# Optimization experiments

Hardware: AMD Instinct MI355X
Metric: run time of the kernel (lower is better)

Reference implementation:

```python
import jax, jax.numpy as jnp
import numpy as np

B, S, D, H = 4, 1024, 1024, 16
DK = D // H
EPS = 1e-6

def setup_inputs() -> dict:
    key = jax.random.key(0)
    ks = jax.random.split(key, 7)
    scale = 1.0 / np.sqrt(D)
    return {
        "query": jax.random.normal(ks[0], (B, S, D), jnp.float32),
        "key": jax.random.normal(ks[1], (B, S, D), jnp.float32),
        "value": jax.random.normal(ks[2], (B, S, D), jnp.float32),
        "Wq": jax.random.normal(ks[3], (D, D), jnp.float32) * scale,
        "Wk": jax.random.normal(ks[4], (D, D), jnp.float32) * scale,
        "Wv": jax.random.normal(ks[5], (D, D), jnp.float32) * scale,
        "Wo": jax.random.normal(ks[6], (D, D), jnp.float32) * scale,
        "ln_gamma": jnp.ones((D,), jnp.float32),
        "ln_beta": jnp.zeros((D,), jnp.float32),
    }

def reference(query, key, value, Wq, Wk, Wv, Wo, ln_gamma, ln_beta):
    residual = query
    # projections (torch Linear: x @ W.T); reshape to [B,H,S,DK]
    def proj(x, W):
        y = jnp.einsum('bsd,ed->bse', x, W)
        return y.reshape(B, S, H, DK).transpose(0, 2, 1, 3)
    q, k, v = proj(query, Wq), proj(key, Wk), proj(value, Wv)
    scores = jnp.einsum('bhqd,bhkd->bhqk', q, k) / jnp.sqrt(jnp.float32(DK))
    p = jax.nn.softmax(scores, axis=-1)
    x = jnp.einsum('bhqk,bhkd->bhqd', p, v)
    x = x.transpose(0, 2, 1, 3).reshape(B, S, D)
    x = jnp.einsum('bsd,ed->bse', x, Wo)
    x = x + residual
    mu = jnp.mean(x, axis=-1, keepdims=True)
    var = jnp.var(x, axis=-1, keepdims=True)
    x = (x - mu) / jnp.sqrt(var + EPS) * ln_gamma + ln_beta
    return x
```

## Files before the change

### kernel.cpp

```cpp
#include <hip/hip_runtime.h>
#include <hip/hip_bf16.h>

#define B_ 4
#define S_ 1024
#define D_ 1024
#define H_ 16
#define DK_ 64
#define MROWS (B_*S_)

typedef short bf16x8 __attribute__((ext_vector_type(8)));
typedef float f32x4 __attribute__((ext_vector_type(4)));
typedef unsigned short u16;
typedef unsigned u32;
typedef u16 u16x4 __attribute__((ext_vector_type(4)));

__device__ __forceinline__ u16 f2bf(float f) {
    union { float f; unsigned u; } v; v.f = f;
    unsigned u = v.u;
    u += 0x7fff + ((u >> 16) & 1);
    return (u16)(u >> 16);
}

__device__ __forceinline__ void gld_lds16(const u16* gp, u16* lp) {
    __builtin_amdgcn_global_load_lds(
        (const __attribute__((address_space(1))) void*)gp,
        (__attribute__((address_space(3))) void*)lp,
        16, 0, 0);
}

__global__ __launch_bounds__(256) void pack_bf16(
    const float* __restrict__ q, const float* __restrict__ k, const float* __restrict__ v,
    const float* __restrict__ wq, const float* __restrict__ wk,
    const float* __restrict__ wv, const float* __restrict__ wo,
    u16* __restrict__ act_dst, u16* __restrict__ w_dst)
{
    const int NACT = 3 * MROWS * D_;
    const int NW   = 4 * D_ * D_;
    for (int c = blockIdx.x * blockDim.x + threadIdx.x;
         c < (NACT + NW) / 4; c += gridDim.x * blockDim.x) {
        int e = c * 4;
        const float* s; u16* d;
        if (e < NACT) {
            int t = e >> 22;
            int off = e & (4194304 - 1);
            s = (t == 0 ? q : t == 1 ? k : v) + off;
            d = act_dst + e;
        } else {
            int e2 = e - NACT;
            int t = e2 >> 20;
            int off = e2 & (1048576 - 1);
            s = (t == 0 ? wq : t == 1 ? wk : t == 2 ? wv : wo) + off;
            d = w_dst + e2;
        }
        float4 tv = *(const float4*)s;
        u16x4 o; o[0]=f2bf(tv.x); o[1]=f2bf(tv.y); o[2]=f2bf(tv.z); o[3]=f2bf(tv.w);
        *(u16x4*)d = o;
    }
}

template<int BM, bool EPI_RESID, bool VT>
__global__ __launch_bounds__(256) void gemm_fast(
    const u16* __restrict__ Ab, const u16* __restrict__ Wb,
    u16* __restrict__ Cb, float* __restrict__ Cf, const float* __restrict__ resid)
{
    constexpr int WN = (BM == 128) ? 2 : 4;
    constexpr int WCOLS = 128 / WN;
    constexpr int NR = WCOLS / 16;
    __shared__ u16 ldsA[BM * 64];
    __shared__ u16 ldsB[128 * 64];

    const int gx = gridDim.x, gy = gridDim.y, gz = gridDim.z;
    const int nwg = gx * gy * gz;
    const int flat = blockIdx.x + gx * (blockIdx.y + gy * blockIdx.z);
    const int f = (flat & 7) * (nwg >> 3) + (flat >> 3);
    const int bx = f % gx;
    const int rem = f / gx;
    const int by = rem % gy;
    const int z = rem / gy;

    Ab += (size_t)z * MROWS * D_;
    Wb += (size_t)z * D_ * D_;
    const u16* CbT = Cb + (EPI_RESID ? 0 : (size_t)z * MROWS * D_);
    u16* Cbz = (u16*)CbT;

    const int tid = threadIdx.x, lane = tid & 63, wid = tid >> 6;
    const int wr = (BM == 128) ? (wid >> 1) : 0;
    const int wc = (BM == 128) ? (wid & 1) : wid;
    const int m0 = by * BM, n0 = bx * 128;
    const int wbase = wid * 64;

    f32x4 acc[4][NR] = {};

    for (int kt = 0; kt < 1024; kt += 64) {
        __syncthreads();
        #pragma unroll
        for (int j = 0; j < BM / 32; ++j) {
            int ch = j * 256 + tid;
            int row = ch >> 3, c8 = (ch & 7) ^ (row & 7);
            gld_lds16(Ab + (size_t)(m0 + row) * 1024 + kt + c8 * 8,
                      &ldsA[(j * 256 + wbase) * 8]);
        }
        #pragma unroll
        for (int j = 0; j < 4; ++j) {
            int ch = j * 256 + tid;
            int row = ch >> 3, c8 = (ch & 7) ^ (row & 7);
            gld_lds16(Wb + (size_t)(n0 + row) * 1024 + kt + c8 * 8,
                      &ldsB[(j * 256 + wbase) * 8]);
        }
        __syncthreads();

        #pragma unroll
        for (int ks = 0; ks < 2; ++ks) {
            const int cb = ks * 32 + (lane >> 4) * 8;
            bf16x8 af[4], bfr[NR];
            #pragma unroll
            for (int m = 0; m < 4; ++m) {
                int row = wr * 64 + m * 16 + (lane & 15);
                af[m] = *(const bf16x8*)(&ldsA[row * 64 + (cb ^ ((row & 7) << 3))]);
            }
            #pragma unroll
            for (int n = 0; n < NR; ++n) {
                int row = wc * WCOLS + n * 16 + (lane & 15);
                bfr[n] = *(const bf16x8*)(&ldsB[row * 64 + (cb ^ ((row & 7) << 3))]);
            }
            #pragma unroll
            for (int m = 0; m < 4; ++m)
                #pragma unroll
                for (int n = 0; n < NR; ++n)
                    acc[m][n] = __builtin_amdgcn_mfma_f32_16x16x32_bf16(
                        af[m], bfr[n], acc[m][n], 0, 0, 0);
        }
    }

    if (VT && z == 2) {
        #pragma unroll
        for (int m = 0; m < 4; ++m)
            #pragma unroll
            for (int n = 0; n < NR; ++n) {
                u16x4 o;
                #pragma unroll
                for (int r = 0; r < 4; ++r) o[r] = f2bf(acc[m][n][r]);
                int grow = m0 + wr * 64 + m * 16 + (lane >> 4) * 4;
                int gcol = n0 + wc * WCOLS + n * 16 + (lane & 15);
                *(u16x4*)(&Cbz[(size_t)gcol * MROWS + grow]) = o;
            }
    } else {
        #pragma unroll
        for (int m = 0; m < 4; ++m)
            #pragma unroll
            for (int n = 0; n < NR; ++n)
                #pragma unroll
                for (int r = 0; r < 4; ++r) {
                    int grow = m0 + wr * 64 + m * 16 + (lane >> 4) * 4 + r;
                    int gcol = n0 + wc * WCOLS + n * 16 + (lane & 15);
                    if (EPI_RESID)
                        Cf[(size_t)grow * 1024 + gcol] = acc[m][n][r] + resid[(size_t)grow * 1024 + gcol];
                    else
                        Cbz[(size_t)grow * 1024 + gcol] = f2bf(acc[m][n][r]);
                }
    }
}

template<bool A_BF16, bool EPI_RESID>
__global__ __launch_bounds__(256) void gemm_bt(
    const void* __restrict__ Av, const float* __restrict__ Bw,
    u16* __restrict__ Cb, float* __restrict__ Cf,
    const float* __restrict__ resid, int M, int N, int K)
{
    __shared__ u16 lds[2][128 * 64];
    const int tid  = threadIdx.x;
    const int lane = tid & 63;
    const int wid  = tid >> 6;
    const int wr = wid >> 1, wc = wid & 1;
    const int m0 = blockIdx.y * 128, n0 = blockIdx.x * 128;

    f32x4 acc[4][4] = {};

    for (int kt = 0; kt < K; kt += 64) {
        #pragma unroll
        for (int j = 0; j < 8; ++j) {
            int idx4 = tid + 256 * j;
            int r = idx4 >> 4;
            int c = (idx4 & 15) * 4;
            u16x4 aw, bw;
            if (A_BF16) {
                const u16* Ab2 = (const u16*)Av;
                aw = *(const u16x4*)(Ab2 + (size_t)(m0 + r) * K + kt + c);
            } else {
                const float* Af = (const float*)Av;
                float4 t = *(const float4*)(Af + (size_t)(m0 + r) * K + kt + c);
                aw[0] = f2bf(t.x); aw[1] = f2bf(t.y); aw[2] = f2bf(t.z); aw[3] = f2bf(t.w);
            }
            {
                float4 t = *(const float4*)(Bw + (size_t)(n0 + r) * K + kt + c);
                bw[0] = f2bf(t.x); bw[1] = f2bf(t.y); bw[2] = f2bf(t.z); bw[3] = f2bf(t.w);
            }
            int sa = r * 64 + (c ^ ((r & 7) << 3));
            *(u16x4*)(&lds[0][sa]) = aw;
            *(u16x4*)(&lds[1][sa]) = bw;
        }
        __syncthreads();
        #pragma unroll
        for (int ks = 0; ks < 2; ++ks) {
            const int cb = ks * 32 + (lane >> 4) * 8;
            bf16x8 af[4], bfr[4];
            #pragma unroll
            for (int m = 0; m < 4; ++m) {
                int row = wr * 64 + m * 16 + (lane & 15);
                af[m] = *(const bf16x8*)(&lds[0][row * 64 + (cb ^ ((row & 7) << 3))]);
            }
            #pragma unroll
            for (int n = 0; n < 4; ++n) {
                int row = wc * 64 + n * 16 + (lane & 15);
                bfr[n] = *(const bf16x8*)(&lds[1][row * 64 + (cb ^ ((row & 7) << 3))]);
            }
            #pragma unroll
            for (int m = 0; m < 4; ++m)
                #pragma unroll
                for (int n = 0; n < 4; ++n)
                    acc[m][n] = __builtin_amdgcn_mfma_f32_16x16x32_bf16(
                        af[m], bfr[n], acc[m][n], 0, 0, 0);
        }
        __syncthreads();
    }

    #pragma unroll
    for (int m = 0; m < 4; ++m)
        #pragma unroll
        for (int n = 0; n < 4; ++n)
            #pragma unroll
            for (int r = 0; r < 4; ++r) {
                int grow = m0 + wr * 64 + m * 16 + (lane >> 4) * 4 + r;
                int gcol = n0 + wc * 64 + n * 16 + (lane & 15);
                float v = acc[m][n][r];
                if (EPI_RESID)
                    Cf[(size_t)grow * N + gcol] = v + resid[(size_t)grow * N + gcol];
                else
                    Cb[(size_t)grow * N + gcol] = f2bf(v);
            }
}

__global__ __launch_bounds__(512, 4) void attn_fwd6(
    const u16* __restrict__ Qg, const u16* __restrict__ Kg,
    const u16* __restrict__ Vt, u16* __restrict__ Og)
{
    __shared__ u16 ks2[64 * 64];
    __shared__ u16 vsT[64 * 64];
    __shared__ u16 ps[128 * 64];

    const int tid = threadIdx.x, lane = tid & 63, w = tid >> 6;
    const int g = lane >> 4, ql = lane & 15;

    const int bid = blockIdx.x;
    const int f = (bid & 7) * 64 + (bid >> 3);
    const int qt = f & 7, h = (f >> 3) & 15, b = f >> 7;
    const int q0 = qt * 128;
    const size_t rbase = (size_t)b * S_;
    const int cb0 = h * DK_;

    bf16x8 qb[2];
    {
        const u16* qp = Qg + (rbase + q0 + w * 16 + ql) * D_ + cb0 + 8 * g;
        qb[0] = *(const bf16x8*)(qp);
        qb[1] = *(const bf16x8*)(qp + 32);
    }

    auto stage_k = [&](int kv0) {
        int row = tid >> 3, c8 = (tid & 7) ^ (row & 7);
        gld_lds16(Kg + (rbase + kv0 + row) * D_ + cb0 + c8 * 8, &ks2[w * 512]);
    };
    auto stage_v = [&](int kv0) {
        int row = tid >> 3, c8 = (tid & 7) ^ (row & 7);
        gld_lds16(Vt + (size_t)(cb0 + row) * MROWS + rbase + kv0 + c8 * 8, &vsT[w * 512]);
    };

    stage_k(0);
    stage_v(0);
    __syncthreads();

    float mrow = -1e30f, lrow = 0.f;
    f32x4 xacc[4] = {};

    for (int jt = 0; jt < 16; ++jt) {
        f32x4 sacc[4] = {};
        __builtin_amdgcn_s_setprio(1);
        #pragma unroll
        for (int ks = 0; ks < 2; ++ks) {
            #pragma unroll
            for (int n = 0; n < 4; ++n) {
                int krow = n * 16 + ql;
                int c = 32 * ks + 8 * g;
                bf16x8 kf = *(const bf16x8*)(&ks2[krow * 64 + (c ^ ((krow & 7) << 3))]);
                sacc[n] = __builtin_amdgcn_mfma_f32_16x16x32_bf16(kf, qb[ks], sacc[n], 0, 0, 0);
            }
        }
        __builtin_amdgcn_s_setprio(0);

        __syncthreads();
        if (jt < 15) stage_k((jt + 1) * 64);

        float mt = sacc[0][0];
        #pragma unroll
        for (int n = 0; n < 4; ++n)
            #pragma unroll
            for (int r = 0; r < 4; ++r) mt = fmaxf(mt, sacc[n][r]);
        mt = fmaxf(mt, __shfl_xor(mt, 16));
        mt = fmaxf(mt, __shfl_xor(mt, 32));
        if (!__all(mt * 0.125f - mrow <= 8.f)) {
            float mnew = fmaxf(mrow, mt * 0.125f);
            float alpha = __expf(mrow - mnew);
            mrow = mnew;
            lrow *= alpha;
            #pragma unroll
            for (int r = 0; r < 4; ++r) {
                float a_r = __shfl(alpha, 4 * g + r);
                #pragma unroll
                for (int n2 = 0; n2 < 4; ++n2) xacc[n2][r] *= a_r;
            }
        }
        float rsum = 0.f;
        u16 pb[16];
        #pragma unroll
        for (int n = 0; n < 4; ++n)
            #pragma unroll
            for (int r = 0; r < 4; ++r) {
                float p = __expf(sacc[n][r] * 0.125f - mrow);
                rsum += p;
                pb[n * 4 + r] = f2bf(p);
            }
        rsum += __shfl_xor(rsum, 16);
        rsum += __shfl_xor(rsum, 32);
        lrow += rsum;

        {
            const int q = w * 16 + ql;
            #pragma unroll
            for (int n = 0; n < 4; ++n) {
                int c = 16 * n + 4 * g;
                *(u16x4*)(&ps[q * 64 + (c ^ ((q & 7) << 3))]) = *(const u16x4*)(&pb[n * 4]);
            }
        }
        asm volatile("s_waitcnt lgkmcnt(0)" ::: "memory");
        __builtin_amdgcn_sched_barrier(0);

        bf16x8 pa[2];
        {
            const int q = w * 16 + ql;
            #pragma unroll
            for (int ks = 0; ks < 2; ++ks) {
                int c = 32 * ks + 8 * g;
                pa[ks] = *(const bf16x8*)(&ps[q * 64 + (c ^ ((q & 7) << 3))]);
            }
        }

        __builtin_amdgcn_s_setprio(1);
        #pragma unroll
        for (int ks = 0; ks < 2; ++ks)
            #pragma unroll
            for (int n2 = 0; n2 < 4; ++n2) {
                int vrow = n2 * 16 + ql;
                int c2 = 32 * ks + 8 * g;
                bf16x8 bv = *(const bf16x8*)(&vsT[vrow * 64 + (c2 ^ ((vrow & 7) << 3))]);
                xacc[n2] = __builtin_amdgcn_mfma_f32_16x16x32_bf16(pa[ks], bv, xacc[n2], 0, 0, 0);
            }
        __builtin_amdgcn_s_setprio(0);

        __syncthreads();
        if (jt < 15) stage_v((jt + 1) * 64);
    }

    float linv[4];
    #pragma unroll
    for (int r = 0; r < 4; ++r) linv[r] = 1.f / __shfl(lrow, 4 * g + r);
    #pragma unroll
    for (int n2 = 0; n2 < 4; ++n2)
        #pragma unroll
        for (int r = 0; r < 4; ++r) {
            int qrow = q0 + w * 16 + 4 * g + r;
            int col = cb0 + n2 * 16 + ql;
            Og[(rbase + qrow) * D_ + col] = f2bf(xacc[n2][r] * linv[r]);
        }
}

__global__ __launch_bounds__(256) void attn_fwd(
    const u16* __restrict__ Qg, const u16* __restrict__ Kg,
    const u16* __restrict__ Vg, u16* __restrict__ Og)
{
    __shared__ u16 qs[64 * 64], ks2[64 * 64], vt[64 * 64], ps[64 * 64];
    const int tid = threadIdx.x, lane = tid & 63, w = tid >> 6;
    const int b = blockIdx.z, h = blockIdx.y, q0 = blockIdx.x * 64;
    const size_t rbase = (size_t)b * S_;
    const int cb0 = h * DK_;

    #pragma unroll
    for (int j = 0; j < 4; ++j) {
        int idx4 = tid + 256 * j;
        int r = idx4 >> 4, c = (idx4 & 15) * 4;
        u16x4 t = *(const u16x4*)(Qg + (rbase + q0 + r) * D_ + cb0 + c);
        *(u16x4*)(&qs[r * 64 + (c ^ ((r & 7) << 3))]) = t;
    }

    float mrow[4], lrow[4];
    f32x4 xacc[4] = {};
    #pragma unroll
    for (int r = 0; r < 4; ++r) { mrow[r] = -1e30f; lrow[r] = 0.f; }

    for (int jt = 0; jt < 16; ++jt) {
        const int kv0 = jt * 64;
        __syncthreads();
        #pragma unroll
        for (int j = 0; j < 4; ++j) {
            int idx4 = tid + 256 * j;
            int r = idx4 >> 4, c = (idx4 & 15) * 4;
            u16x4 t = *(const u16x4*)(Kg + (rbase + kv0 + r) * D_ + cb0 + c);
            *(u16x4*)(&ks2[r * 64 + (c ^ ((r & 7) << 3))]) = t;
            u16x4 tv = *(const u16x4*)(Vg + (rbase + kv0 + r) * D_ + cb0 + c);
            #pragma unroll
            for (int jj = 0; jj < 4; ++jj) {
                int d = c + jj;
                vt[d * 64 + (r ^ ((d & 7) << 3))] = tv[jj];
            }
        }
        __syncthreads();

        f32x4 sacc[4] = {};
        #pragma unroll
        for (int ks = 0; ks < 2; ++ks) {
            const int cb = ks * 32 + (lane >> 4) * 8;
            int qrow = w * 16 + (lane & 15);
            bf16x8 aq = *(const bf16x8*)(&qs[qrow * 64 + (cb ^ ((qrow & 7) << 3))]);
            #pragma unroll
            for (int n = 0; n < 4; ++n) {
                int krow = n * 16 + (lane & 15);
                bf16x8 bk = *(const bf16x8*)(&ks2[krow * 64 + (cb ^ ((krow & 7) << 3))]);
                sacc[n] = __builtin_amdgcn_mfma_f32_16x16x32_bf16(aq, bk, sacc[n], 0, 0, 0);
            }
        }

        #pragma unroll
        for (int r = 0; r < 4; ++r) {
            float mx = fmaxf(fmaxf(sacc[0][r], sacc[1][r]),
                             fmaxf(sacc[2][r], sacc[3][r]));
            mx = fmaxf(mx, __shfl_xor(mx, 1));
            mx = fmaxf(mx, __shfl_xor(mx, 2));
            mx = fmaxf(mx, __shfl_xor(mx, 4));
            mx = fmaxf(mx, __shfl_xor(mx, 8));
            float mnew = fmaxf(mrow[r], mx * 0.125f);
            float alpha = __expf(mrow[r] - mnew);
            float p[4], rsum = 0.f;
            #pragma unroll
            for (int n = 0; n < 4; ++n) { p[n] = __expf(sacc[n][r] * 0.125f - mnew); rsum += p[n]; }
            rsum += __shfl_xor(rsum, 1);
            rsum += __shfl_xor(rsum, 2);
            rsum += __shfl_xor(rsum, 4);
            rsum += __shfl_xor(rsum, 8);
            lrow[r] = lrow[r] * alpha + rsum;
            mrow[r] = mnew;
            int qrow = w * 16 + (lane >> 4) * 4 + r;
            #pragma unroll
            for (int n = 0; n < 4; ++n) {
                xacc[n][r] *= alpha;
                int col = n * 16 + (lane & 15);
                ps[qrow * 64 + (col ^ ((qrow & 7) << 3))] = f2bf(p[n]);
            }
        }
        __syncthreads();

        #pragma unroll
        for (int ks = 0; ks < 2; ++ks) {
            const int cb = ks * 32 + (lane >> 4) * 8;
            int prow = w * 16 + (lane & 15);
            bf16x8 ap = *(const bf16x8*)(&ps[prow * 64 + (cb ^ ((prow & 7) << 3))]);
            #pragma unroll
            for (int n = 0; n < 4; ++n) {
                int vrow = n * 16 + (lane & 15);
                bf16x8 bv = *(const bf16x8*)(&vt[vrow * 64 + (cb ^ ((vrow & 7) << 3))]);
                xacc[n] = __builtin_amdgcn_mfma_f32_16x16x32_bf16(ap, bv, xacc[n], 0, 0, 0);
            }
        }
    }

    #pragma unroll
    for (int n = 0; n < 4; ++n)
        #pragma unroll
        for (int r = 0; r < 4; ++r) {
            int qrow = q0 + w * 16 + (lane >> 4) * 4 + r;
            int col = cb0 + n * 16 + (lane & 15);
            Og[(rbase + qrow) * D_ + col] = f2bf(xacc[n][r] / lrow[r]);
        }
}

__global__ __launch_bounds__(256) void ln_inplace(
    float* __restrict__ Y, const float* __restrict__ g, const float* __restrict__ bt)
{
    __shared__ float red[2][4];
    const int row = blockIdx.x, tid = threadIdx.x;
    float4 v = *(const float4*)(Y + (size_t)row * D_ + tid * 4);
    float s = v.x + v.y + v.z + v.w;
    float q = v.x * v.x + v.y * v.y + v.z * v.z + v.w * v.w;
    #pragma unroll
    for (int m = 1; m < 64; m <<= 1) { s += __shfl_xor(s, m); q += __shfl_xor(q, m); }
    const int w = tid >> 6, lane = tid & 63;
    if (lane == 0) { red[0][w] = s; red[1][w] = q; }
    __syncthreads();
    s = red[0][0] + red[0][1] + red[0][2] + red[0][3];
    q = red[1][0] + red[1][1] + red[1][2] + red[1][3];
    float mu = s * (1.f / 1024.f);
    float var = q * (1.f / 1024.f) - mu * mu;
    float rstd = rsqrtf(var + 1e-6f);
    float4 gv = *(const float4*)(g + tid * 4);
    float4 bv = *(const float4*)(bt + tid * 4);
    v.x = (v.x - mu) * rstd * gv.x + bv.x;
    v.y = (v.y - mu) * rstd * gv.y + bv.y;
    v.z = (v.z - mu) * rstd * gv.z + bv.z;
    v.w = (v.w - mu) * rstd * gv.w + bv.w;
    *(float4*)(Y + (size_t)row * D_ + tid * 4) = v;
}

extern "C" void kernel_launch(void* const* d_in, const int* in_sizes, int n_in,
                              void* d_out, int out_size, void* d_ws, size_t ws_size,
                              hipStream_t stream)
{
    const float* query = (const float*)d_in[0];
    const float* key   = (const float*)d_in[1];
    const float* value = (const float*)d_in[2];
    const float* Wq    = (const float*)d_in[3];
    const float* Wk    = (const float*)d_in[4];
    const float* Wv    = (const float*)d_in[5];
    const float* Wo    = (const float*)d_in[6];
    const float* gamma = (const float*)d_in[7];
    const float* beta  = (const float*)d_in[8];
    float* out = (float*)d_out;

    const size_t ACT = (size_t)MROWS * D_;
    const size_t WSZ = (size_t)D_ * D_;
    const size_t NEED = (3 * ACT + 4 * WSZ + 3 * ACT) * 2;

    if (ws_size >= NEED) {
        u16* actb = (u16*)d_ws;
        u16* wb   = actb + 3 * ACT;
        u16* pb   = wb + 4 * WSZ;
        u16* Ap   = actb;

        pack_bf16<<<2048, 256, 0, stream>>>(query, key, value, Wq, Wk, Wv, Wo, actb, wb);
        gemm_fast<128, false, true><<<dim3(8, 32, 3), 256, 0, stream>>>(actb, wb, pb, nullptr, nullptr);
        attn_fwd6<<<512, 512, 0, stream>>>(pb, pb + ACT, pb + 2 * ACT, Ap);
        gemm_fast<64, true, false><<<dim3(8, 64, 1), 256, 0, stream>>>(Ap, wb + 3 * WSZ, nullptr, out, query);
        ln_inplace<<<MROWS, 256, 0, stream>>>(out, gamma, beta);
    } else {
        u16* Qp = (u16*)d_ws;
        u16* Kp = Qp + ACT;
        u16* Vp = Kp + ACT;
        u16* Ap = Vp + ACT;
        dim3 gg(D_ / 128, MROWS / 128);
        gemm_bt<false, false><<<gg, 256, 0, stream>>>(query, Wq, Qp, nullptr, nullptr, MROWS, D_, D_);
        gemm_bt<false, false><<<gg, 256, 0, stream>>>(key,   Wk, Kp, nullptr, nullptr, MROWS, D_, D_);
        gemm_bt<false, false><<<gg, 256, 0, stream>>>(value, Wv, Vp, nullptr, nullptr, MROWS, D_, D_);
        attn_fwd<<<dim3(S_ / 64, H_, B_), 256, 0, stream>>>(Qp, Kp, Vp, Ap);
        gemm_bt<true, true><<<gg, 256, 0, stream>>>(Ap, Wo, nullptr, out, query, MROWS, D_, D_);
        ln_inplace<<<MROWS, 256, 0, stream>>>(out, gamma, beta);
    }
}
```

Measured before the change: 119.6 us.

## Double-buffer B tile and prefetch next K-step during MFMA compute in GEMM

Restructures the GEMM main loop so each warp reads its A fragments into registers first. After a barrier, it issues async global-to-LDS loads for the next K-step: A goes into the now-free single A buffer and B into the alternate half of a double-buffered B tile. The MFMAs on the current tile then run while those loads are in flight. The aim is to hide global load latency behind compute, at the cost of extra LDS for the second B buffer, more registers held for A fragments, and an extra barrier per iteration.

New measurement: 114.9 us. 3.9% less time.

```diff
diff --git a/kernel.cpp b/kernel.cpp
--- a/kernel.cpp
+++ b/kernel.cpp
@@ -67,7 +67,7 @@
     constexpr int WCOLS = 128 / WN;
     constexpr int NR = WCOLS / 16;
     __shared__ u16 ldsA[BM * 64];
-    __shared__ u16 ldsB[128 * 64];
+    __shared__ u16 ldsB[2][128 * 64];
 
     const int gx = gridDim.x, gy = gridDim.y, gz = gridDim.z;
     const int nwg = gx * gy * gz;
@@ -89,10 +89,8 @@
     const int m0 = by * BM, n0 = bx * 128;
     const int wbase = wid * 64;
 
-    f32x4 acc[4][NR] = {};
-
-    for (int kt = 0; kt < 1024; kt += 64) {
-        __syncthreads();
+    auto stageA = [&](int it) {
+        const int kt = it * 64;
         #pragma unroll
         for (int j = 0; j < BM / 32; ++j) {
             int ch = j * 256 + tid;
@@ -100,36 +98,63 @@
             gld_lds16(Ab + (size_t)(m0 + row) * 1024 + kt + c8 * 8,
                       &ldsA[(j * 256 + wbase) * 8]);
         }
+    };
+    auto stageB = [&](int p, int it) {
+        const int kt = it * 64;
         #pragma unroll
         for (int j = 0; j < 4; ++j) {
             int ch = j * 256 + tid;
             int row = ch >> 3, c8 = (ch & 7) ^ (row & 7);
             gld_lds16(Wb + (size_t)(n0 + row) * 1024 + kt + c8 * 8,
-                      &ldsB[(j * 256 + wbase) * 8]);
-        }
-        __syncthreads();
-
+                      &ldsB[p][(j * 256 + wbase) * 8]);
+        }
+    };
+
+    f32x4 acc[4][NR] = {};
+
+    stageA(0);
+    stageB(0, 0);
+    __syncthreads();
+
+    for (int it = 0; it < 16; ++it) {
+        const int bcur = it & 1;
+
+        bf16x8 af[2][4];
         #pragma unroll
         for (int ks = 0; ks < 2; ++ks) {
             const int cb = ks * 32 + (lane >> 4) * 8;
-            bf16x8 af[4], bfr[NR];
             #pragma unroll
             for (int m = 0; m < 4; ++m) {
                 int row = wr * 64 + m * 16 + (lane & 15);
-                af[m] = *(const bf16x8*)(&ldsA[row * 64 + (cb ^ ((row & 7) << 3))]);
-            }
+                af[ks][m] = *(const bf16x8*)(&ldsA[row * 64 + (cb ^ ((row & 7) << 3))]);
+            }
+        }
+        __syncthreads();
+
+        if (it < 15) {
+            stageA(it + 1);
+            stageB(bcur ^ 1, it + 1);
+        }
+        __builtin_amdgcn_sched_barrier(0);
+
+        #pragma unroll
+        for (int ks = 0; ks < 2; ++ks) {
+            const int cb = ks * 32 + (lane >> 4) * 8;
+            bf16x8 bfr[NR];
             #pragma unroll
             for (int n = 0; n < NR; ++n) {
                 int row = wc * WCOLS + n * 16 + (lane & 15);
-                bfr[n] = *(const bf16x8*)(&ldsB[row * 64 + (cb ^ ((row & 7) << 3))]);
+                bfr[n] = *(const bf16x8*)(&ldsB[bcur][row * 64 + (cb ^ ((row & 7) << 3))]);
             }
             #pragma unroll
             for (int m = 0; m < 4; ++m)
                 #pragma unroll
                 for (int n = 0; n < NR; ++n)
                     acc[m][n] = __builtin_amdgcn_mfma_f32_16x16x32_bf16(
-                        af[m], bfr[n], acc[m][n], 0, 0, 0);
-        }
+                        af[ks][m], bfr[n], acc[m][n], 0, 0, 0);
+        }
+
+        __syncthreads();
     }
 
     if (VT && z == 2) {
```
